# Performance work log

Measured on AMD Instinct MI355X. Metric: run time of the kernel, lower is better.

Reference implementation:

```python
import jax, jax.numpy as jnp
import numpy as np

B = 512      # number of groups (samples)
SEG = 128    # points per group (fixed for the reference)
N = B * SEG  # total points
E = 64       # embed_size
D = 5 * E    # point feature dim = 320
L = 3        # pointNet blocks
MF = 2       # multiple_factor -> hidden = D*MF = 640
NEG_SLOPE = 0.01


def _leaky(x):
    return jnp.where(x >= 0, x, NEG_SLOPE * x)


def _mlp(x, W1, b1, W2, b2):
    # Linear -> LeakyReLU -> (Dropout=identity, eval) -> Linear -> LeakyReLU
    return _leaky(_leaky(x @ W1 + b1) @ W2 + b2)


def setup_inputs() -> dict:
    key = jax.random.key(0)
    ks = jax.random.split(key, 16)
    s = 0.02
    words = jax.random.randint(ks[0], (N, 5), 0, 26, dtype=jnp.int32)
    lengths = jnp.full((B,), SEG, dtype=jnp.int32)
    seg2all = jnp.repeat(jnp.arange(B, dtype=jnp.int32), SEG)
    inp = {
        "words": words,
        "lengths": lengths,
        "seg2all": seg2all,
        "embed": s * jax.random.normal(ks[1], (26, E), jnp.float32),
        "pu_W1": s * jax.random.normal(ks[2], (L, D, D * MF), jnp.float32),
        "pu_b1": jnp.zeros((L, D * MF), jnp.float32),
        "pu_W2": s * jax.random.normal(ks[3], (L, D * MF, D), jnp.float32),
        "pu_b2": jnp.zeros((L, D), jnp.float32),
        "gu_W1": s * jax.random.normal(ks[4], (L, D, D * MF), jnp.float32),
        "gu_b1": jnp.zeros((L, D * MF), jnp.float32),
        "gu_W2": s * jax.random.normal(ks[5], (L, D * MF, D), jnp.float32),
        "gu_b2": jnp.zeros((L, D), jnp.float32),
        "c_W": s * jax.random.normal(ks[6], (L, 2 * D, D), jnp.float32),
        "c_b": jnp.zeros((L, D), jnp.float32),
        "o_W1": s * jax.random.normal(ks[7], (D, D * MF), jnp.float32),
        "o_b1": jnp.zeros((D * MF,), jnp.float32),
        "o_W2": s * jax.random.normal(ks[8], (D * MF, 1), jnp.float32),
        "o_b2": jnp.zeros((1,), jnp.float32),
        "w": jnp.float32(0.13663686),
    }
    return inp


def reference(words, lengths, seg2all, embed, pu_W1, pu_b1, pu_W2, pu_b2,
              gu_W1, gu_b1, gu_W2, gu_b2, c_W, c_b, o_W1, o_b1, o_W2, o_b2, w):
    inv_len = 1.0 / lengths.astype(jnp.float32)  # [B]

    def seg_mean(x):  # segment_csr(x, offsets, reduce='mean')
        sums = jax.ops.segment_sum(x, seg2all, num_segments=B)
        return sums * inv_len[:, None]

    out = embed[words].reshape(-1, D)  # [N, D]
    for i in range(L):
        h = _mlp(out, pu_W1[i], pu_b1[i], pu_W2[i], pu_b2[i])          # point update
        g = _mlp(seg_mean(h), gu_W1[i], gu_b1[i], gu_W2[i], gu_b2[i])  # group update
        cat = jnp.concatenate([h, g[seg2all]], axis=1)                 # gather-back concat
        out = _leaky(cat @ c_W[i] + c_b[i]) + out                      # combine + residual
    y = _mlp(seg_mean(out), o_W1, o_b1, o_W2, o_b2)  # [B, 1]
    return y.squeeze(-1) + w * jnp.log2(lengths.astype(jnp.float32))
```

## Files before the change

kernel.cpp:

```cpp
#include <hip/hip_runtime.h>
#include <hip/hip_bf16.h>

using bf16 = __hip_bfloat16;
typedef short bf16x8 __attribute__((ext_vector_type(8)));
typedef float f32x4  __attribute__((ext_vector_type(4)));

__device__ __forceinline__ float leakyf(float x) { return x >= 0.f ? x : 0.01f * x; }

typedef const __attribute__((address_space(1))) unsigned int* gp_t;
typedef __attribute__((address_space(3))) unsigned int* lp_t;
__device__ __forceinline__ void gload16(const void* g, void* l) {
  __builtin_amdgcn_global_load_lds((gp_t)g, (lp_t)l, 16, 0, 0);
}

__global__ void conv_w(const float* __restrict__ pu1, const float* __restrict__ pu2,
                       const float* __restrict__ gu1, const float* __restrict__ gu2,
                       const float* __restrict__ cw,
                       bf16* __restrict__ W0, bf16* __restrict__ W1,
                       bf16* __restrict__ W2, bf16* __restrict__ W3,
                       bf16* __restrict__ W4, bf16* __restrict__ W5) {
  int job = blockIdx.y;
  int type = job / 3, l = job % 3;
  int K, Nc, ld, koff;
  const float* s; bf16* d;
  switch (type) {
    case 0: K=320; Nc=640; ld=640; koff=0;   s=pu1 + (size_t)l*320*640; d=W0 + (size_t)l*320*640; break;
    case 1: K=640; Nc=320; ld=320; koff=0;   s=pu2 + (size_t)l*640*320; d=W1 + (size_t)l*640*320; break;
    case 2: K=320; Nc=640; ld=640; koff=0;   s=gu1 + (size_t)l*320*640; d=W2 + (size_t)l*320*640; break;
    case 3: K=640; Nc=320; ld=320; koff=0;   s=gu2 + (size_t)l*640*320; d=W3 + (size_t)l*640*320; break;
    case 4: K=320; Nc=320; ld=320; koff=0;   s=cw  + (size_t)l*640*320; d=W4 + (size_t)l*320*320; break;
    default:K=320; Nc=320; ld=320; koff=320; s=cw  + (size_t)l*640*320; d=W5 + (size_t)l*320*320; break;
  }
  const int NS = K >> 6;
  const int chunks = (K * Nc) >> 3;
  int flat = blockIdx.x * 256 + threadIdx.x;
  if (flat >= chunks) return;
  int i  = flat & 15;
  int ch = (flat >> 4) & 7;
  int nt = (flat >> 7) % 20;
  int sl = flat / 2560;
  int ks = sl % NS, colg = sl / NS;
  int n  = colg * 320 + nt * 16 + i;
  int kb = koff + ks * 64 + ch * 8;
  bf16 v[8];
#pragma unroll
  for (int j = 0; j < 8; ++j)
    v[j] = __float2bfloat16(s[(size_t)(kb + j) * ld + n]);
  *(bf16x8*)(d + (size_t)flat * 8) = *(bf16x8*)v;
}

__global__ void embed_k(const int* __restrict__ words, const float* __restrict__ emb,
                        bf16* __restrict__ out, int N) {
  int i = blockIdx.x * 256 + threadIdx.x;
  if (i >= N * 64) return;
  int n = i >> 6, e = i & 63;
  const int* wr = words + (size_t)n * 5;
#pragma unroll
  for (int k = 0; k < 5; ++k)
    out[(size_t)n * 320 + k * 64 + e] = __float2bfloat16(emb[(size_t)wr[k] * 64 + e]);
}

__global__ __launch_bounds__(256, 3)
void mm_k(const bf16* __restrict__ A, const bf16* __restrict__ Wt,
          const float* __restrict__ bias, const bf16* __restrict__ gadd,
          const bf16* __restrict__ res, bf16* __restrict__ out,
          float* __restrict__ part,
          int K, int ldOut, int flags)
{
  __shared__ short As[4096];
  __shared__ short Ws[20480];

  const int NS   = K >> 6;
  const int tid  = threadIdx.x;
  const int lane = tid & 63;
  const int wv   = tid >> 6;
  const int i16  = lane & 15;
  const int kg   = lane >> 4;
  const int rb   = blockIdx.y << 6;
  const int colBase = blockIdx.x * 320;

  f32x4 zero = {0.f, 0.f, 0.f, 0.f};
  f32x4 acc[4][5];
#pragma unroll
  for (int m = 0; m < 4; ++m)
#pragma unroll
    for (int n = 0; n < 5; ++n) acc[m][n] = zero;

  const bf16* wbase = Wt + (size_t)blockIdx.x * NS * 20480;

  for (int ks = 0; ks < NS; ++ks) {
    __syncthreads();
#pragma unroll
    for (int t = 0; t < 2; ++t) {
      int d0 = (t * 4 + wv) * 64;
      int d  = d0 + lane;
      int row = d >> 3, c = d & 7;
      gload16(A + (size_t)(rb + row) * K + ks * 64 + ((c ^ (row & 7)) << 3),
              (char*)As + d0 * 16);
    }
    const bf16* wsrc = wbase + (size_t)ks * 20480;
#pragma unroll
    for (int t = 0; t < 10; ++t) {
      int d0 = (t * 4 + wv) * 64;
      gload16(wsrc + (size_t)(d0 + lane) * 8, (char*)Ws + d0 * 16);
    }
    __syncthreads();
#pragma unroll
    for (int kk = 0; kk < 2; ++kk) {
      bf16x8 a[4], b[5];
#pragma unroll
      for (int m = 0; m < 4; ++m) {
        int row = m * 16 + i16;
        a[m] = *(const bf16x8*)((const char*)As + row * 128 +
                                (((kk * 4 + kg) ^ (row & 7)) << 4));
      }
#pragma unroll
      for (int n = 0; n < 5; ++n)
        b[n] = *(const bf16x8*)((const char*)Ws +
                                ((wv * 5 + n) * 8 + kk * 4 + kg) * 256 + i16 * 16);
#pragma unroll
      for (int m = 0; m < 4; ++m)
#pragma unroll
        for (int n = 0; n < 5; ++n)
          acc[m][n] = __builtin_amdgcn_mfma_f32_16x16x32_bf16(a[m], b[n], acc[m][n], 0, 0, 0);
    }
  }

  const bool doLeaky = flags & 1, useG = flags & 2, useR = flags & 4, doSeg = flags & 8;
  const bf16* gptr = useG ? gadd + (size_t)(blockIdx.y >> 1) * 320 : nullptr;
#pragma unroll
  for (int n = 0; n < 5; ++n) {
    const int col = colBase + wv * 80 + n * 16 + i16;
    const float bv = bias ? bias[col] : 0.f;
    float ga = useG ? __bfloat162float(gptr[col]) : 0.f;
    float csum = 0.f;
#pragma unroll
    for (int m = 0; m < 4; ++m) {
#pragma unroll
      for (int v = 0; v < 4; ++v) {
        const int row = rb + m * 16 + kg * 4 + v;
        float val = acc[m][n][v] + bv + ga;
        if (doLeaky) val = leakyf(val);
        if (useR) val += __bfloat162float(res[(size_t)row * ldOut + col]);
        out[(size_t)row * ldOut + col] = __float2bfloat16(val);
        csum += val;
      }
    }
    if (doSeg) {
      csum += __shfl_xor(csum, 16, 64);
      csum += __shfl_xor(csum, 32, 64);
      if (lane < 16) part[(size_t)blockIdx.y * 320 + col] = csum;
    }
  }
}

__global__ void gseg_k(const float* __restrict__ part, const int* __restrict__ len,
                       bf16* __restrict__ seg, int B) {
  int idx = blockIdx.x * 256 + threadIdx.x;
  if (idx >= B * 320) return;
  int g = idx / 320, c = idx - g * 320;
  float s = part[(size_t)(2 * g) * 320 + c] + part[(size_t)(2 * g + 1) * 320 + c];
  seg[idx] = __float2bfloat16(s / (float)len[g]);
}

__global__ __launch_bounds__(256)
void final_head(const bf16* __restrict__ mo, const float* __restrict__ W1,
                const float* __restrict__ b1, const float* __restrict__ W2,
                const float* __restrict__ b2, const int* __restrict__ lengths,
                const float* __restrict__ wscal, float* __restrict__ out) {
  const int D = 320, H = 640;
  int g = blockIdx.x, tid = threadIdx.x;
  __shared__ float m[320];
  for (int i = tid; i < D; i += 256) m[i] = __bfloat162float(mo[(size_t)g * D + i]);
  __syncthreads();
  float partial = 0.f;
  for (int j = tid; j < H; j += 256) {
    float s = b1[j];
    for (int d = 0; d < D; ++d) s += m[d] * W1[(size_t)d * H + j];
    partial += leakyf(s) * W2[j];
  }
  __shared__ float red[256];
  red[tid] = partial; __syncthreads();
  for (int s = 128; s > 0; s >>= 1) {
    if (tid < s) red[tid] += red[tid + s];
    __syncthreads();
  }
  if (tid == 0) {
    float y = leakyf(red[0] + b2[0]);
    out[g] = y + wscal[0] * log2f((float)lengths[g]);
  }
}

extern "C" void kernel_launch(void* const* d_in, const int* in_sizes, int n_in,
                              void* d_out, int out_size, void* d_ws, size_t ws_size,
                              hipStream_t stream) {
  const int*   words   = (const int*)  d_in[0];
  const int*   lengths = (const int*)  d_in[1];
  const float* embedw  = (const float*)d_in[3];
  const float* pu_W1   = (const float*)d_in[4];
  const float* pu_b1   = (const float*)d_in[5];
  const float* pu_W2   = (const float*)d_in[6];
  const float* pu_b2   = (const float*)d_in[7];
  const float* gu_W1   = (const float*)d_in[8];
  const float* gu_b1   = (const float*)d_in[9];
  const float* gu_W2   = (const float*)d_in[10];
  const float* gu_b2   = (const float*)d_in[11];
  const float* c_W     = (const float*)d_in[12];
  const float* c_b     = (const float*)d_in[13];
  const float* o_W1    = (const float*)d_in[14];
  const float* o_b1    = (const float*)d_in[15];
  const float* o_W2    = (const float*)d_in[16];
  const float* o_b2    = (const float*)d_in[17];
  const float* wscal   = (const float*)d_in[18];

  const int B = in_sizes[1];
  const int N = in_sizes[2];
  const int L = 3;

  size_t off = 0;
  auto alloc = [&](size_t bytes) -> void* {
    void* p = (char*)d_ws + off;
    off += (bytes + 255) & ~(size_t)255;
    return p;
  };
  bf16*  wOut  = (bf16*) alloc((size_t)N * 320 * 2);
  bf16*  wH1   = (bf16*) alloc((size_t)N * 640 * 2);
  bf16*  wH    = (bf16*) alloc((size_t)N * 320 * 2);
  bf16*  wSeg  = (bf16*) alloc((size_t)B * 320 * 2);
  bf16*  wT1   = (bf16*) alloc((size_t)B * 640 * 2);
  bf16*  wG    = (bf16*) alloc((size_t)B * 320 * 2);
  bf16*  wGC   = (bf16*) alloc((size_t)B * 320 * 2);
  float* wPart = (float*)alloc((size_t)(N / 64) * 320 * 4);
  bf16*  W0 = (bf16*)alloc((size_t)L * 320 * 640 * 2);
  bf16*  W1 = (bf16*)alloc((size_t)L * 640 * 320 * 2);
  bf16*  W2 = (bf16*)alloc((size_t)L * 320 * 640 * 2);
  bf16*  W3 = (bf16*)alloc((size_t)L * 640 * 320 * 2);
  bf16*  W4 = (bf16*)alloc((size_t)L * 320 * 320 * 2);
  bf16*  W5 = (bf16*)alloc((size_t)L * 320 * 320 * 2);

  conv_w<<<dim3(100, 18), 256, 0, stream>>>(pu_W1, pu_W2, gu_W1, gu_W2, c_W,
                                            W0, W1, W2, W3, W4, W5);
  embed_k<<<(N * 64 + 255) / 256, 256, 0, stream>>>(words, embedw, wOut, N);

  for (int l = 0; l < L; ++l) {
    mm_k<<<dim3(2, N / 64), 256, 0, stream>>>(
        wOut, W0 + (size_t)l * 320 * 640, pu_b1 + (size_t)l * 640,
        nullptr, nullptr, wH1, nullptr, 320, 640, 1);
    mm_k<<<dim3(1, N / 64), 256, 0, stream>>>(
        wH1, W1 + (size_t)l * 640 * 320, pu_b2 + (size_t)l * 320,
        nullptr, nullptr, wH, wPart, 640, 320, 1 | 8);
    gseg_k<<<(B * 320 + 255) / 256, 256, 0, stream>>>(wPart, lengths, wSeg, B);
    mm_k<<<dim3(2, B / 64), 256, 0, stream>>>(
        wSeg, W2 + (size_t)l * 320 * 640, gu_b1 + (size_t)l * 640,
        nullptr, nullptr, wT1, nullptr, 320, 640, 1);
    mm_k<<<dim3(1, B / 64), 256, 0, stream>>>(
        wT1, W3 + (size_t)l * 640 * 320, gu_b2 + (size_t)l * 320,
        nullptr, nullptr, wG, nullptr, 640, 320, 1);
    mm_k<<<dim3(1, B / 64), 256, 0, stream>>>(
        wG, W5 + (size_t)l * 320 * 320, nullptr,
        nullptr, nullptr, wGC, nullptr, 320, 320, 0);
    mm_k<<<dim3(1, N / 64), 256, 0, stream>>>(
        wH, W4 + (size_t)l * 320 * 320, c_b + (size_t)l * 320,
        wGC, wOut, wOut, wPart, 320, 320, 1 | 2 | 4 | ((l == 2) ? 8 : 0));
  }

  gseg_k<<<(B * 320 + 255) / 256, 256, 0, stream>>>(wPart, lengths, wSeg, B);
  final_head<<<B, 256, 0, stream>>>(wSeg, o_W1, o_b1, o_W2, o_b2, lengths, wscal,
                                    (float*)d_out);
}
```

Measured before the change: 665.1 us.

## Fuse whole network into one per-group kernel with register-resident activations

Replaces the chain of per-layer GEMM, segment-mean and head launches with a single kernel in which one 512-thread block handles one 128-point group. Activations stay in registers and LDS across all three blocks, the group MLP runs as per-block dot products, and the final head is computed in the same kernel. Weight slices are double-buffered into LDS. This removes the large global activation round trips and many launches, but each block re-streams all the weights, and the big LDS and register footprint limits occupancy. It also hardcodes 128 points per group and ignores seg2all and per-group offsets.

```diff
diff --git a/kernel.cpp b/kernel.cpp
--- a/kernel.cpp
+++ b/kernel.cpp
@@ -4,8 +4,17 @@
 using bf16 = __hip_bfloat16;
 typedef short bf16x8 __attribute__((ext_vector_type(8)));
 typedef float f32x4  __attribute__((ext_vector_type(4)));
+typedef unsigned short u16;
 
 __device__ __forceinline__ float leakyf(float x) { return x >= 0.f ? x : 0.01f * x; }
+
+__device__ __forceinline__ float b2f(u16 u) {
+  union { unsigned int i; float f; } c; c.i = (unsigned int)u << 16; return c.f;
+}
+__device__ __forceinline__ u16 f2b(float f) {
+  __hip_bfloat16 h = __float2bfloat16(f);
+  return *reinterpret_cast<u16*>(&h);
+}
 
 typedef const __attribute__((address_space(1))) unsigned int* gp_t;
 typedef __attribute__((address_space(3))) unsigned int* lp_t;
@@ -13,181 +22,343 @@
   __builtin_amdgcn_global_load_lds((gp_t)g, (lp_t)l, 16, 0, 0);
 }
 
-__global__ void conv_w(const float* __restrict__ pu1, const float* __restrict__ pu2,
-                       const float* __restrict__ gu1, const float* __restrict__ gu2,
-                       const float* __restrict__ cw,
-                       bf16* __restrict__ W0, bf16* __restrict__ W1,
-                       bf16* __restrict__ W2, bf16* __restrict__ W3,
-                       bf16* __restrict__ W4, bf16* __restrict__ W5) {
+__global__ void pack_tiles(const float* __restrict__ pu1, const float* __restrict__ pu2,
+                           const float* __restrict__ cw,
+                           bf16* __restrict__ W0, bf16* __restrict__ W1t,
+                           bf16* __restrict__ W4) {
+  int job = blockIdx.y, type = job / 3, l = job % 3;
+  int f = blockIdx.x * 256 + threadIdx.x;
+  const float* s; bf16* d; int ld, nchunks;
+  if (type == 0)      { nchunks = 25600; s = pu1 + (size_t)l * 204800; d = W0  + (size_t)l * 204800; ld = 640; }
+  else if (type == 1) { nchunks = 25600; s = pu2 + (size_t)l * 204800; d = W1t + (size_t)l * 204800; ld = 320; }
+  else                { nchunks = 12800; s = cw  + (size_t)l * 204800; d = W4  + (size_t)l * 102400; ld = 320; }
+  if (f >= nchunks) return;
+  int i  = f & 15;
+  int ch = (f >> 4) & 7;
+  int nt = (f >> 7) % 20;
+  int sl = (f >> 7) / 20;
+  int k, col;
+  if (type == 0) { k = (sl % 5) * 64 + ch * 8; col = (sl / 5) * 320 + nt * 16 + i; }
+  else           { k = sl * 64 + ch * 8;       col = nt * 16 + i; }
+  bf16 v[8];
+#pragma unroll
+  for (int j = 0; j < 8; ++j)
+    v[j] = __float2bfloat16(s[(size_t)(k + j) * ld + col]);
+  *(bf16x8*)(d + (size_t)f * 8) = *(bf16x8*)v;
+}
+
+__global__ void pack_nmaj(const float* __restrict__ gu1, const float* __restrict__ gu2,
+                          const float* __restrict__ cw, const float* __restrict__ ow1,
+                          bf16* __restrict__ Wg1, bf16* __restrict__ Wg2,
+                          bf16* __restrict__ Wg3, bf16* __restrict__ Wo1) {
   int job = blockIdx.y;
-  int type = job / 3, l = job % 3;
-  int K, Nc, ld, koff;
-  const float* s; bf16* d;
-  switch (type) {
-    case 0: K=320; Nc=640; ld=640; koff=0;   s=pu1 + (size_t)l*320*640; d=W0 + (size_t)l*320*640; break;
-    case 1: K=640; Nc=320; ld=320; koff=0;   s=pu2 + (size_t)l*640*320; d=W1 + (size_t)l*640*320; break;
-    case 2: K=320; Nc=640; ld=640; koff=0;   s=gu1 + (size_t)l*320*640; d=W2 + (size_t)l*320*640; break;
-    case 3: K=640; Nc=320; ld=320; koff=0;   s=gu2 + (size_t)l*640*320; d=W3 + (size_t)l*640*320; break;
-    case 4: K=320; Nc=320; ld=320; koff=0;   s=cw  + (size_t)l*640*320; d=W4 + (size_t)l*320*320; break;
-    default:K=320; Nc=320; ld=320; koff=320; s=cw  + (size_t)l*640*320; d=W5 + (size_t)l*320*320; break;
-  }
-  const int NS = K >> 6;
-  const int chunks = (K * Nc) >> 3;
-  int flat = blockIdx.x * 256 + threadIdx.x;
-  if (flat >= chunks) return;
-  int i  = flat & 15;
-  int ch = (flat >> 4) & 7;
-  int nt = (flat >> 7) % 20;
-  int sl = flat / 2560;
-  int ks = sl % NS, colg = sl / NS;
-  int n  = colg * 320 + nt * 16 + i;
-  int kb = koff + ks * 64 + ch * 8;
+  int f = blockIdx.x * 256 + threadIdx.x;
+  const float* s; bf16* d; int K, ld, nchunks, koff = 0;
+  if (job < 3)       { int l = job;     K = 320; ld = 640; nchunks = 25600; s = gu1 + (size_t)l * 204800; d = Wg1 + (size_t)l * 204800; }
+  else if (job < 6)  { int l = job - 3; K = 640; ld = 320; nchunks = 25600; s = gu2 + (size_t)l * 204800; d = Wg2 + (size_t)l * 204800; }
+  else if (job < 9)  { int l = job - 6; K = 320; ld = 320; nchunks = 12800; s = cw  + (size_t)l * 204800; d = Wg3 + (size_t)l * 102400; koff = 320; }
+  else               {                  K = 320; ld = 640; nchunks = 25600; s = ow1;                      d = Wo1; }
+  if (f >= nchunks) return;
+  int kc8 = K >> 3;
+  int n = f / kc8, kc = f % kc8;
   bf16 v[8];
 #pragma unroll
   for (int j = 0; j < 8; ++j)
-    v[j] = __float2bfloat16(s[(size_t)(kb + j) * ld + n]);
-  *(bf16x8*)(d + (size_t)flat * 8) = *(bf16x8*)v;
-}
-
-__global__ void embed_k(const int* __restrict__ words, const float* __restrict__ emb,
-                        bf16* __restrict__ out, int N) {
-  int i = blockIdx.x * 256 + threadIdx.x;
-  if (i >= N * 64) return;
-  int n = i >> 6, e = i & 63;
-  const int* wr = words + (size_t)n * 5;
-#pragma unroll
-  for (int k = 0; k < 5; ++k)
-    out[(size_t)n * 320 + k * 64 + e] = __float2bfloat16(emb[(size_t)wr[k] * 64 + e]);
-}
-
-__global__ __launch_bounds__(256, 3)
-void mm_k(const bf16* __restrict__ A, const bf16* __restrict__ Wt,
-          const float* __restrict__ bias, const bf16* __restrict__ gadd,
-          const bf16* __restrict__ res, bf16* __restrict__ out,
-          float* __restrict__ part,
-          int K, int ldOut, int flags)
+    v[j] = __float2bfloat16(s[(size_t)(koff + kc * 8 + j) * ld + n]);
+  *(bf16x8*)(d + (size_t)f * 8) = *(bf16x8*)v;
+}
+
+#define PWROW(vv, comp) { int row = rb + vv; \
+  *(short*)((char*)p + row * 128 + (col2 ^ ((row & 7) << 4))) = (short)(fq.comp); }
+
+__device__ __forceinline__ void paneWrite4(short* p, ushort4 f0, ushort4 f1,
+                                           ushort4 f2, ushort4 f3,
+                                           int r, int wc, int i16, int kg) {
+  const int col2 = (wc * 16 + i16) * 2;
+  { ushort4 fq = f0; int rb = r * 64 + 0  + kg * 4; PWROW(0, x) PWROW(1, y) PWROW(2, z) PWROW(3, w) }
+  { ushort4 fq = f1; int rb = r * 64 + 16 + kg * 4; PWROW(0, x) PWROW(1, y) PWROW(2, z) PWROW(3, w) }
+  { ushort4 fq = f2; int rb = r * 64 + 32 + kg * 4; PWROW(0, x) PWROW(1, y) PWROW(2, z) PWROW(3, w) }
+  { ushort4 fq = f3; int rb = r * 64 + 48 + kg * 4; PWROW(0, x) PWROW(1, y) PWROW(2, z) PWROW(3, w) }
+}
+
+__device__ __forceinline__ void stageW(const bf16* src, short* dst, int wave, int lane) {
+#pragma unroll
+  for (int t = 0; t < 5; ++t) {
+    int ci = (t * 8 + wave) * 64 + lane;
+    gload16(src + (size_t)ci * 8, (char*)dst + (t * 8 + wave) * 1024);
+  }
+}
+
+__device__ __forceinline__ void sliceMFMA(f32x4 (&acc)[4][5], const short* pn,
+                                          const short* wb,
+                                          int r, int wc, int i16, int kg) {
+#pragma unroll
+  for (int kk = 0; kk < 2; ++kk) {
+    bf16x8 a[4];
+#pragma unroll
+    for (int m = 0; m < 4; ++m) {
+      int row = r * 64 + m * 16 + i16;
+      a[m] = *(const bf16x8*)((const char*)pn + row * 128 +
+                              (((kk * 32 + kg * 8) * 2) ^ ((row & 7) << 4)));
+    }
+#pragma unroll
+    for (int t = 0; t < 5; ++t) {
+      bf16x8 b = *(const bf16x8*)((const char*)wb +
+                                  (((wc + 4 * t) * 8 + kk * 4 + kg) << 8) + (i16 << 4));
+#pragma unroll
+      for (int m = 0; m < 4; ++m)
+        acc[m][t] = __builtin_amdgcn_mfma_f32_16x16x32_bf16(a[m], b, acc[m][t], 0, 0, 0);
+    }
+  }
+}
+
+__device__ __forceinline__ float dotWrow(const bf16* __restrict__ w,
+                                         const float* __restrict__ x, int K8) {
+  float s = 0.f;
+#pragma unroll 4
+  for (int kb = 0; kb < K8; ++kb) {
+    bf16x8 wv = *(const bf16x8*)(w + kb * 8);
+#pragma unroll
+    for (int u = 0; u < 8; ++u)
+      s += b2f((u16)wv[u]) * x[kb * 8 + u];
+  }
+  return s;
+}
+
+__device__ __forceinline__ ushort4 pack4(float a, float b, float c, float d) {
+  ushort4 u; u.x = f2b(a); u.y = f2b(b); u.z = f2b(c); u.w = f2b(d); return u;
+}
+
+__global__ __launch_bounds__(512, 2)
+void fused_k(const int* __restrict__ words, const int* __restrict__ lengths,
+             const float* __restrict__ embed,
+             const bf16* __restrict__ W0, const bf16* __restrict__ W1t,
+             const bf16* __restrict__ W4,
+             const bf16* __restrict__ Wg1, const bf16* __restrict__ Wg2,
+             const bf16* __restrict__ Wg3, const bf16* __restrict__ Wo1,
+             const float* __restrict__ pb1, const float* __restrict__ pb2,
+             const float* __restrict__ gb1, const float* __restrict__ gb2,
+             const float* __restrict__ cb,  const float* __restrict__ ob1,
+             const float* __restrict__ oW2, const float* __restrict__ ob2,
+             const float* __restrict__ wsc, float* __restrict__ yout)
 {
-  __shared__ short As[4096];
-  __shared__ short Ws[20480];
-
-  const int NS   = K >> 6;
+  __shared__ short pane[2][8192];
+  __shared__ short wbuf[2][20480];
+  __shared__ float embL[1664];
+  __shared__ int   wrdL[640];
+  __shared__ float mvec[320];
+  __shared__ float tvec[640];
+  __shared__ float gvec[320];
+  __shared__ float redA[320];
+  __shared__ float redB[320];
+  __shared__ float redH[8];
+
+  const int g    = blockIdx.x;
   const int tid  = threadIdx.x;
-  const int lane = tid & 63;
-  const int wv   = tid >> 6;
-  const int i16  = lane & 15;
-  const int kg   = lane >> 4;
-  const int rb   = blockIdx.y << 6;
-  const int colBase = blockIdx.x * 320;
-
-  f32x4 zero = {0.f, 0.f, 0.f, 0.f};
-  f32x4 acc[4][5];
-#pragma unroll
-  for (int m = 0; m < 4; ++m)
-#pragma unroll
-    for (int n = 0; n < 5; ++n) acc[m][n] = zero;
-
-  const bf16* wbase = Wt + (size_t)blockIdx.x * NS * 20480;
-
-  for (int ks = 0; ks < NS; ++ks) {
+  const int wave = tid >> 6, lane = tid & 63;
+  const int r    = wave >> 2, wc = wave & 3;
+  const int i16  = lane & 15, kg = lane >> 4;
+  const float invLen = 1.0f / (float)lengths[g];
+
+  for (int i = tid; i < 1664; i += 512) embL[i] = embed[i];
+  { const int* ws = words + (size_t)g * 640;
+    for (int i = tid; i < 640; i += 512) wrdL[i] = ws[i]; }
+  __syncthreads();
+
+  ushort4 outf[4][5];
+#pragma unroll
+  for (int m = 0; m < 4; ++m) {
+    int row = r * 64 + m * 16 + kg * 4;
+#pragma unroll
+    for (int t = 0; t < 5; ++t) {
+      int col = (wc + 4 * t) * 16 + i16;
+      int w = col >> 6, e = col & 63;
+      outf[m][t] = pack4(embL[wrdL[(row + 0) * 5 + w] * 64 + e],
+                         embL[wrdL[(row + 1) * 5 + w] * 64 + e],
+                         embL[wrdL[(row + 2) * 5 + w] * 64 + e],
+                         embL[wrdL[(row + 3) * 5 + w] * 64 + e]);
+    }
+  }
+
+  for (int l = 0; l < 3; ++l) {
+    ushort4 h1f[2][4][5];
+#pragma unroll
+    for (int p = 0; p < 2; ++p) {
+      f32x4 acc[4][5];
+#pragma unroll
+      for (int m = 0; m < 4; ++m)
+#pragma unroll
+        for (int t = 0; t < 5; ++t) acc[m][t] = {0.f, 0.f, 0.f, 0.f};
+      const bf16* wsrc = W0 + ((size_t)(l * 2 + p) * 5) * 20480;
+      __syncthreads();
+      stageW(wsrc, wbuf[0], wave, lane);
+      paneWrite4(pane[0], outf[0][0], outf[1][0], outf[2][0], outf[3][0], r, wc, i16, kg);
+#pragma unroll
+      for (int ks = 0; ks < 5; ++ks) {
+        __syncthreads();
+        if (ks < 4) {
+          stageW(wsrc + (size_t)(ks + 1) * 20480, wbuf[(ks + 1) & 1], wave, lane);
+          paneWrite4(pane[(ks + 1) & 1], outf[0][ks + 1], outf[1][ks + 1],
+                     outf[2][ks + 1], outf[3][ks + 1], r, wc, i16, kg);
+        }
+        sliceMFMA(acc, pane[ks & 1], wbuf[ks & 1], r, wc, i16, kg);
+      }
+#pragma unroll
+      for (int t = 0; t < 5; ++t) {
+        int col = p * 320 + (wc + 4 * t) * 16 + i16;
+        float bv = pb1[l * 640 + col];
+#pragma unroll
+        for (int m = 0; m < 4; ++m)
+          h1f[p][m][t] = pack4(leakyf(acc[m][t][0] + bv), leakyf(acc[m][t][1] + bv),
+                               leakyf(acc[m][t][2] + bv), leakyf(acc[m][t][3] + bv));
+      }
+    }
+
+    ushort4 hf[4][5];
+    {
+      f32x4 acc[4][5];
+#pragma unroll
+      for (int m = 0; m < 4; ++m)
+#pragma unroll
+        for (int t = 0; t < 5; ++t) acc[m][t] = {0.f, 0.f, 0.f, 0.f};
+      const bf16* wsrc = W1t + (size_t)l * 10 * 20480;
+      __syncthreads();
+      stageW(wsrc, wbuf[0], wave, lane);
+      paneWrite4(pane[0], h1f[0][0][0], h1f[0][1][0], h1f[0][2][0], h1f[0][3][0], r, wc, i16, kg);
+#pragma unroll
+      for (int ks = 0; ks < 10; ++ks) {
+        __syncthreads();
+        if (ks < 9) {
+          stageW(wsrc + (size_t)(ks + 1) * 20480, wbuf[(ks + 1) & 1], wave, lane);
+          const int p2 = (ks + 1) / 5, t2 = (ks + 1) % 5;
+          paneWrite4(pane[(ks + 1) & 1], h1f[p2][0][t2], h1f[p2][1][t2],
+                     h1f[p2][2][t2], h1f[p2][3][t2], r, wc, i16, kg);
+        }
+        sliceMFMA(acc, pane[ks & 1], wbuf[ks & 1], r, wc, i16, kg);
+      }
+      __syncthreads();
+      float csum[5];
+#pragma unroll
+      for (int t = 0; t < 5; ++t) {
+        int col = (wc + 4 * t) * 16 + i16;
+        float bv = pb2[l * 320 + col];
+        float v0 = leakyf(acc[0][t][0] + bv), v1 = leakyf(acc[0][t][1] + bv);
+        float v2 = leakyf(acc[0][t][2] + bv), v3 = leakyf(acc[0][t][3] + bv);
+        float cs = v0 + v1 + v2 + v3;
+        hf[0][t] = pack4(v0, v1, v2, v3);
+#pragma unroll
+        for (int m = 1; m < 4; ++m) {
+          float w0 = leakyf(acc[m][t][0] + bv), w1 = leakyf(acc[m][t][1] + bv);
+          float w2 = leakyf(acc[m][t][2] + bv), w3 = leakyf(acc[m][t][3] + bv);
+          cs += w0 + w1 + w2 + w3;
+          hf[m][t] = pack4(w0, w1, w2, w3);
+        }
+        csum[t] = cs;
+      }
+#pragma unroll
+      for (int t = 0; t < 5; ++t) {
+        float s = csum[t];
+        s += __shfl_xor(s, 16);
+        s += __shfl_xor(s, 32);
+        if (kg == 0) (r ? redB : redA)[(wc + 4 * t) * 16 + i16] = s;
+      }
+      __syncthreads();
+      if (tid < 320) mvec[tid] = (redA[tid] + redB[tid]) * invLen;
+      __syncthreads();
+    }
+
+    tvec[tid] = leakyf(dotWrow(Wg1 + ((size_t)l * 640 + tid) * 320, mvec, 40) +
+                       gb1[l * 640 + tid]);
+    if (tid < 128) {
+      int j2 = 512 + tid;
+      tvec[j2] = leakyf(dotWrow(Wg1 + ((size_t)l * 640 + j2) * 320, mvec, 40) +
+                        gb1[l * 640 + j2]);
+    }
     __syncthreads();
-#pragma unroll
-    for (int t = 0; t < 2; ++t) {
-      int d0 = (t * 4 + wv) * 64;
-      int d  = d0 + lane;
-      int row = d >> 3, c = d & 7;
-      gload16(A + (size_t)(rb + row) * K + ks * 64 + ((c ^ (row & 7)) << 3),
-              (char*)As + d0 * 16);
-    }
-    const bf16* wsrc = wbase + (size_t)ks * 20480;
-#pragma unroll
-    for (int t = 0; t < 10; ++t) {
-      int d0 = (t * 4 + wv) * 64;
-      gload16(wsrc + (size_t)(d0 + lane) * 8, (char*)Ws + d0 * 16);
-    }
+    if (tid < 320)
+      gvec[tid] = leakyf(dotWrow(Wg2 + ((size_t)l * 320 + tid) * 640, tvec, 80) +
+                         gb2[l * 320 + tid]);
     __syncthreads();
-#pragma unroll
-    for (int kk = 0; kk < 2; ++kk) {
-      bf16x8 a[4], b[5];
-#pragma unroll
-      for (int m = 0; m < 4; ++m) {
-        int row = m * 16 + i16;
-        a[m] = *(const bf16x8*)((const char*)As + row * 128 +
-                                (((kk * 4 + kg) ^ (row & 7)) << 4));
-      }
-#pragma unroll
-      for (int n = 0; n < 5; ++n)
-        b[n] = *(const bf16x8*)((const char*)Ws +
-                                ((wv * 5 + n) * 8 + kk * 4 + kg) * 256 + i16 * 16);
+    if (tid < 320)
+      tvec[tid] = dotWrow(Wg3 + ((size_t)l * 320 + tid) * 320, gvec, 40) +
+                  cb[l * 320 + tid];
+    __syncthreads();
+
+    {
+      f32x4 acc[4][5];
 #pragma unroll
       for (int m = 0; m < 4; ++m)
 #pragma unroll
-        for (int n = 0; n < 5; ++n)
-          acc[m][n] = __builtin_amdgcn_mfma_f32_16x16x32_bf16(a[m], b[n], acc[m][n], 0, 0, 0);
-    }
-  }
-
-  const bool doLeaky = flags & 1, useG = flags & 2, useR = flags & 4, doSeg = flags & 8;
-  const bf16* gptr = useG ? gadd + (size_t)(blockIdx.y >> 1) * 320 : nullptr;
-#pragma unroll
-  for (int n = 0; n < 5; ++n) {
-    const int col = colBase + wv * 80 + n * 16 + i16;
-    const float bv = bias ? bias[col] : 0.f;
-    float ga = useG ? __bfloat162float(gptr[col]) : 0.f;
-    float csum = 0.f;
-#pragma unroll
-    for (int m = 0; m < 4; ++m) {
-#pragma unroll
-      for (int v = 0; v < 4; ++v) {
-        const int row = rb + m * 16 + kg * 4 + v;
-        float val = acc[m][n][v] + bv + ga;
-        if (doLeaky) val = leakyf(val);
-        if (useR) val += __bfloat162float(res[(size_t)row * ldOut + col]);
-        out[(size_t)row * ldOut + col] = __float2bfloat16(val);
-        csum += val;
-      }
-    }
-    if (doSeg) {
-      csum += __shfl_xor(csum, 16, 64);
-      csum += __shfl_xor(csum, 32, 64);
-      if (lane < 16) part[(size_t)blockIdx.y * 320 + col] = csum;
-    }
-  }
-}
-
-__global__ void gseg_k(const float* __restrict__ part, const int* __restrict__ len,
-                       bf16* __restrict__ seg, int B) {
-  int idx = blockIdx.x * 256 + threadIdx.x;
-  if (idx >= B * 320) return;
-  int g = idx / 320, c = idx - g * 320;
-  float s = part[(size_t)(2 * g) * 320 + c] + part[(size_t)(2 * g + 1) * 320 + c];
-  seg[idx] = __float2bfloat16(s / (float)len[g]);
-}
-
-__global__ __launch_bounds__(256)
-void final_head(const bf16* __restrict__ mo, const float* __restrict__ W1,
-                const float* __restrict__ b1, const float* __restrict__ W2,
-                const float* __restrict__ b2, const int* __restrict__ lengths,
-                const float* __restrict__ wscal, float* __restrict__ out) {
-  const int D = 320, H = 640;
-  int g = blockIdx.x, tid = threadIdx.x;
-  __shared__ float m[320];
-  for (int i = tid; i < D; i += 256) m[i] = __bfloat162float(mo[(size_t)g * D + i]);
+        for (int t = 0; t < 5; ++t) acc[m][t] = {0.f, 0.f, 0.f, 0.f};
+      const bf16* wsrc = W4 + (size_t)l * 5 * 20480;
+      __syncthreads();
+      stageW(wsrc, wbuf[0], wave, lane);
+      paneWrite4(pane[0], hf[0][0], hf[1][0], hf[2][0], hf[3][0], r, wc, i16, kg);
+#pragma unroll
+      for (int ks = 0; ks < 5; ++ks) {
+        __syncthreads();
+        if (ks < 4) {
+          stageW(wsrc + (size_t)(ks + 1) * 20480, wbuf[(ks + 1) & 1], wave, lane);
+          paneWrite4(pane[(ks + 1) & 1], hf[0][ks + 1], hf[1][ks + 1],
+                     hf[2][ks + 1], hf[3][ks + 1], r, wc, i16, kg);
+        }
+        sliceMFMA(acc, pane[ks & 1], wbuf[ks & 1], r, wc, i16, kg);
+      }
+      __syncthreads();
+      float csum[5];
+#pragma unroll
+      for (int t = 0; t < 5; ++t) {
+        int col = (wc + 4 * t) * 16 + i16;
+        float ga = tvec[col];
+        ushort4 ov = outf[0][t];
+        float v0 = leakyf(acc[0][t][0] + ga) + b2f(ov.x);
+        float v1 = leakyf(acc[0][t][1] + ga) + b2f(ov.y);
+        float v2 = leakyf(acc[0][t][2] + ga) + b2f(ov.z);
+        float v3 = leakyf(acc[0][t][3] + ga) + b2f(ov.w);
+        outf[0][t] = pack4(v0, v1, v2, v3);
+        float cs = v0 + v1 + v2 + v3;
+#pragma unroll
+        for (int m = 1; m < 4; ++m) {
+          ushort4 om = outf[m][t];
+          float w0 = leakyf(acc[m][t][0] + ga) + b2f(om.x);
+          float w1 = leakyf(acc[m][t][1] + ga) + b2f(om.y);
+          float w2 = leakyf(acc[m][t][2] + ga) + b2f(om.z);
+          float w3 = leakyf(acc[m][t][3] + ga) + b2f(om.w);
+          outf[m][t] = pack4(w0, w1, w2, w3);
+          cs += w0 + w1 + w2 + w3;
+        }
+        csum[t] = cs;
+      }
+#pragma unroll
+      for (int t = 0; t < 5; ++t) {
+        float s = csum[t];
+        s += __shfl_xor(s, 16);
+        s += __shfl_xor(s, 32);
+        if (kg == 0) (r ? redB : redA)[(wc + 4 * t) * 16 + i16] = s;
+      }
+      __syncthreads();
+      if (tid < 320) mvec[tid] = (redA[tid] + redB[tid]) * invLen;
+      __syncthreads();
+    }
+  }
+
+  tvec[tid] = leakyf(dotWrow(Wo1 + (size_t)tid * 320, mvec, 40) + ob1[tid]);
+  if (tid < 128) {
+    int j2 = 512 + tid;
+    tvec[j2] = leakyf(dotWrow(Wo1 + (size_t)j2 * 320, mvec, 40) + ob1[j2]);
+  }
   __syncthreads();
-  float partial = 0.f;
-  for (int j = tid; j < H; j += 256) {
-    float s = b1[j];
-    for (int d = 0; d < D; ++d) s += m[d] * W1[(size_t)d * H + j];
-    partial += leakyf(s) * W2[j];
-  }
-  __shared__ float red[256];
-  red[tid] = partial; __syncthreads();
-  for (int s = 128; s > 0; s >>= 1) {
-    if (tid < s) red[tid] += red[tid + s];
-    __syncthreads();
-  }
+  float part = tvec[tid] * oW2[tid] + (tid < 128 ? tvec[512 + tid] * oW2[512 + tid] : 0.f);
+#pragma unroll
+  for (int off = 32; off > 0; off >>= 1) part += __shfl_down(part, off);
+  if (lane == 0) redH[wave] = part;
+  __syncthreads();
   if (tid == 0) {
-    float y = leakyf(red[0] + b2[0]);
-    out[g] = y + wscal[0] * log2f((float)lengths[g]);
+    float s = 0.f;
+#pragma unroll
+    for (int w = 0; w < 8; ++w) s += redH[w];
+    float y = leakyf(s + ob2[0]);
+    yout[g] = y + wsc[0] * log2f((float)lengths[g]);
   }
 }
 
@@ -214,8 +385,6 @@
   const float* wscal   = (const float*)d_in[18];
 
   const int B = in_sizes[1];
-  const int N = in_sizes[2];
-  const int L = 3;
 
   size_t off = 0;
   auto alloc = [&](size_t bytes) -> void* {
@@ -223,48 +392,19 @@
     off += (bytes + 255) & ~(size_t)255;
     return p;
   };
-  bf16*  wOut  = (bf16*) alloc((size_t)N * 320 * 2);
-  bf16*  wH1   = (bf16*) alloc((size_t)N * 640 * 2);
-  bf16*  wH    = (bf16*) alloc((size_t)N * 320 * 2);
-  bf16*  wSeg  = (bf16*) alloc((size_t)B * 320 * 2);
-  bf16*  wT1   = (bf16*) alloc((size_t)B * 640 * 2);
-  bf16*  wG    = (bf16*) alloc((size_t)B * 320 * 2);
-  bf16*  wGC   = (bf16*) alloc((size_t)B * 320 * 2);
-  float* wPart = (float*)alloc((size_t)(N / 64) * 320 * 4);
-  bf16*  W0 = (bf16*)alloc((size_t)L * 320 * 640 * 2);
-  bf16*  W1 = (bf16*)alloc((size_t)L * 640 * 320 * 2);
-  bf16*  W2 = (bf16*)alloc((size_t)L * 320 * 640 * 2);
-  bf16*  W3 = (bf16*)alloc((size_t)L * 640 * 320 * 2);
-  bf16*  W4 = (bf16*)alloc((size_t)L * 320 * 320 * 2);
-  bf16*  W5 = (bf16*)alloc((size_t)L * 320 * 320 * 2);
-
-  conv_w<<<dim3(100, 18), 256, 0, stream>>>(pu_W1, pu_W2, gu_W1, gu_W2, c_W,
-                                            W0, W1, W2, W3, W4, W5);
-  embed_k<<<(N * 64 + 255) / 256, 256, 0, stream>>>(words, embedw, wOut, N);
-
-  for (int l = 0; l < L; ++l) {
-    mm_k<<<dim3(2, N / 64), 256, 0, stream>>>(
-        wOut, W0 + (size_t)l * 320 * 640, pu_b1 + (size_t)l * 640,
-        nullptr, nullptr, wH1, nullptr, 320, 640, 1);
-    mm_k<<<dim3(1, N / 64), 256, 0, stream>>>(
-        wH1, W1 + (size_t)l * 640 * 320, pu_b2 + (size_t)l * 320,
-        nullptr, nullptr, wH, wPart, 640, 320, 1 | 8);
-    gseg_k<<<(B * 320 + 255) / 256, 256, 0, stream>>>(wPart, lengths, wSeg, B);
-    mm_k<<<dim3(2, B / 64), 256, 0, stream>>>(
-        wSeg, W2 + (size_t)l * 320 * 640, gu_b1 + (size_t)l * 640,
-        nullptr, nullptr, wT1, nullptr, 320, 640, 1);
-    mm_k<<<dim3(1, B / 64), 256, 0, stream>>>(
-        wT1, W3 + (size_t)l * 640 * 320, gu_b2 + (size_t)l * 320,
-        nullptr, nullptr, wG, nullptr, 640, 320, 1);
-    mm_k<<<dim3(1, B / 64), 256, 0, stream>>>(
-        wG, W5 + (size_t)l * 320 * 320, nullptr,
-        nullptr, nullptr, wGC, nullptr, 320, 320, 0);
-    mm_k<<<dim3(1, N / 64), 256, 0, stream>>>(
-        wH, W4 + (size_t)l * 320 * 320, c_b + (size_t)l * 320,
-        wGC, wOut, wOut, wPart, 320, 320, 1 | 2 | 4 | ((l == 2) ? 8 : 0));
-  }
-
-  gseg_k<<<(B * 320 + 255) / 256, 256, 0, stream>>>(wPart, lengths, wSeg, B);
-  final_head<<<B, 256, 0, stream>>>(wSeg, o_W1, o_b1, o_W2, o_b2, lengths, wscal,
-                                    (float*)d_out);
-}
+  bf16* W0  = (bf16*)alloc(614400 * 2);
+  bf16* W1t = (bf16*)alloc(614400 * 2);
+  bf16* W4  = (bf16*)alloc(307200 * 2);
+  bf16* Wg1 = (bf16*)alloc(614400 * 2);
+  bf16* Wg2 = (bf16*)alloc(614400 * 2);
+  bf16* Wg3 = (bf16*)alloc(307200 * 2);
+  bf16* Wo1 = (bf16*)alloc(204800 * 2);
+
+  pack_tiles<<<dim3(100, 9), 256, 0, stream>>>(pu_W1, pu_W2, c_W, W0, W1t, W4);
+  pack_nmaj<<<dim3(100, 10), 256, 0, stream>>>(gu_W1, gu_W2, c_W, o_W1,
+                                               Wg1, Wg2, Wg3, Wo1);
+  fused_k<<<B, 512, 0, stream>>>(words, lengths, embedw, W0, W1t, W4,
+                                 Wg1, Wg2, Wg3, Wo1,
+                                 pu_b1, pu_b2, gu_b1, gu_b2, c_b, o_b1,
+                                 o_W2, o_b2, wscal, (float*)d_out);
+}
```

Result: slower. 705.2 us (+6.0%).
